# Kernel optimization log

Hardware: AMD Instinct MI355X
Metric: run time of the kernel (lower is better)

Reference implementation:

```python
import jax, jax.numpy as jnp
import numpy as np

H = 512

def setup_inputs() -> dict:
    key = jax.random.key(0)
    ks = jax.random.split(key, 10)
    T, B, S = 64, 8, 512
    scale = 1.0 / np.sqrt(H)
    return {
        "attn_dec_state": jax.random.normal(ks[0], (T, B, H), jnp.float32),
        "attn_enc_state": jax.random.normal(ks[1], (S, B, H), jnp.float32),
        "attn_coverage": jax.random.uniform(ks[2], (B, S), jnp.float32),
        "Wq": jax.random.normal(ks[3], (H, H), jnp.float32) * scale,   # linear_query weight (in,out)
        "bq": jnp.zeros((H,), jnp.float32),
        "Wc": jax.random.normal(ks[4], (H, H), jnp.float32) * scale,   # linear_context weight
        "v": jax.random.normal(ks[5], (H,), jnp.float32) * scale,       # v projection H->1
        "Wo": jax.random.normal(ks[6], (2 * H, H), jnp.float32) * scale,  # linear_out weight
        "bo": jnp.zeros((H,), jnp.float32),
        "wcov": jax.random.normal(ks[7], (H,), jnp.float32) * scale,    # linear_cover weight 1->H
    }

def reference(attn_dec_state, attn_enc_state, attn_coverage, Wq, bq, Wc, v, Wo, bo, wcov):
    dec = jnp.transpose(attn_dec_state, (1, 0, 2))   # [B,T,H]
    enc = jnp.transpose(attn_enc_state, (1, 0, 2))   # [B,S,H]
    # coverage: linear_cover(1->H) applied to each scalar, added to enc, then tanh
    enc = jnp.tanh(enc + attn_coverage[:, :, None] * wcov)  # [B,S,H]
    # additive (Bahdanau) score with broadcast-tanh
    a1 = jnp.einsum('bth,hk->btk', dec, Wq) + bq             # [B,T,H]
    a2 = jnp.einsum('bsh,hk->bsk', enc, Wc)                  # [B,S,H]
    scores = jnp.einsum('btsh,h->bts', jnp.tanh(a1[:, :, None, :] + a2[:, None, :, :]), v)  # [B,T,S]
    align = jax.nn.softmax(scores, axis=-1)                  # [B,T,S]
    c = jnp.einsum('bts,bsh->bth', align, enc)               # [B,T,H]
    concat = jnp.concatenate([c, dec], axis=-1)              # [B,T,2H]
    attn_h = jnp.einsum('btd,dk->btk', concat, Wo) + bo      # [B,T,H]
    attn_h = jnp.transpose(attn_h, (1, 0, 2))                # [T,B,H]
    align_out = jnp.transpose(align, (1, 0, 2))              # [T,B,S]
    return attn_h, align_out
```

## Files before the change

### kernel.cpp

```cpp
#include <hip/hip_runtime.h>
#include <cstddef>

static constexpr int TT = 64;
static constexpr int BB = 8;
static constexpr int SS = 512;
static constexpr int HH = 512;

typedef __attribute__((ext_vector_type(8))) short bf16x8;
typedef __attribute__((ext_vector_type(4))) float f32x4;

__device__ __forceinline__ float fast_tanh(float x) {
  float e = __expf(2.0f * x);
  float r = __builtin_amdgcn_rcpf(e + 1.0f);
  return 1.0f - 2.0f * r;
}
__device__ __forceinline__ unsigned short f2bf(float f) {
  unsigned u = __float_as_uint(f);
  unsigned r = (u + 0x7FFFu + ((u >> 16) & 1u)) >> 16;
  return (unsigned short)r;
}

__global__ __launch_bounds__(256)
void k_prep(const float* __restrict__ enc, const float* __restrict__ cov,
            const float* __restrict__ wcov, const float* __restrict__ dec,
            const float* __restrict__ Wq, const float* __restrict__ Wc,
            const float* __restrict__ Wo, const float* __restrict__ v,
            unsigned short* __restrict__ encpb, unsigned short* __restrict__ decb,
            unsigned short* __restrict__ concatb,
            unsigned short* __restrict__ WqT, unsigned short* __restrict__ WcT,
            unsigned short* __restrict__ WoT,
            float* __restrict__ v2, float* __restrict__ Vsum) {
  __shared__ float tile[32][33];
  const int blk = blockIdx.x, tid = threadIdx.x;

  if (blk < 8192) {
    const int idx = blk * 256 + tid;
    const int h = idx & 511;
    const int bs = idx >> 9;
    const int s = bs & 511, b = bs >> 9;
    const float x = enc[(size_t)(s * BB + b) * HH + h] + cov[bs] * wcov[h];
    encpb[idx] = f2bf(fast_tanh(x));
  } else if (blk < 9216) {
    const int idx = (blk - 8192) * 256 + tid;
    const int h = idx & 511, m = idx >> 9;
    const int b = m >> 6, t = m & 63;
    const unsigned short val = f2bf(dec[(size_t)(t * BB + b) * HH + h]);
    decb[idx] = val;
    concatb[(size_t)m * 1024 + 512 + h] = val;
  } else if (blk < 10240) {
    int l = blk - 9216;
    const float* W; unsigned short* WT; int KT;
    if (l < 256)      { W = Wq; WT = WqT; KT = 512; }
    else if (l < 512) { W = Wc; WT = WcT; KT = 512; l -= 256; }
    else              { W = Wo; WT = WoT; KT = 1024; l -= 512; }
    const int n0 = (l & 15) * 32, k0 = (l >> 4) * 32;
    const int r = tid >> 3, c4 = (tid & 7) * 4;
    const float4 w = *(const float4*)(W + (size_t)(k0 + r) * 512 + n0 + c4);
    tile[r][c4 + 0] = w.x; tile[r][c4 + 1] = w.y;
    tile[r][c4 + 2] = w.z; tile[r][c4 + 3] = w.w;
    __syncthreads();
    unsigned short* o = WT + (size_t)(n0 + r) * KT + k0 + c4;
#pragma unroll
    for (int i = 0; i < 4; ++i) o[i] = f2bf(tile[c4 + i][r]);
  } else {
    __shared__ float rb[256];
    const float va = v[tid], vb = v[tid + 256];
    v2[tid] = 2.0f * va;
    v2[tid + 256] = 2.0f * vb;
    rb[tid] = va + vb;
    __syncthreads();
    for (int off = 128; off; off >>= 1) {
      if (tid < off) rb[tid] += rb[tid + off];
      __syncthreads();
    }
    if (tid == 0) Vsum[0] = rb[0];
  }
}

__global__ __launch_bounds__(256)
void k_gemm12(const unsigned short* __restrict__ decb,
              const unsigned short* __restrict__ encpb,
              const unsigned short* __restrict__ WqT,
              const unsigned short* __restrict__ WcT,
              const float* __restrict__ bq,
              float* __restrict__ Ea1, float* __restrict__ Ea2) {
  __shared__ unsigned short As[64][72];
  __shared__ unsigned short Bs[64][72];
  const int tid = threadIdx.x;
  const int w = tid >> 6, lane = tid & 63;

  const bool isA1 = blockIdx.x < 64;
  const int bb = isA1 ? blockIdx.x : blockIdx.x - 64;
  const int n0 = (bb & 7) * 64, m0 = (bb >> 3) * 64;
  const unsigned short* A  = isA1 ? decb : encpb;
  const unsigned short* BT = isA1 ? WqT : WcT;
  float* C = isA1 ? Ea1 : Ea2;

  f32x4 acc[4] = {};
  const int lr = tid >> 2, lk = (tid & 3) * 16;
  const int fm = w * 16 + (lane & 15);
  const int fk = (lane >> 4) * 8;

  for (int k0 = 0; k0 < 512; k0 += 64) {
    const uint4* ga = (const uint4*)(A + (size_t)(m0 + lr) * 512 + k0 + lk);
    const uint4* gb = (const uint4*)(BT + (size_t)(n0 + lr) * 512 + k0 + lk);
    uint4 a0 = ga[0], a1v = ga[1];
    uint4 b0 = gb[0], b1v = gb[1];
    *(uint4*)&As[lr][lk] = a0;
    *(uint4*)&As[lr][lk + 8] = a1v;
    *(uint4*)&Bs[lr][lk] = b0;
    *(uint4*)&Bs[lr][lk + 8] = b1v;
    __syncthreads();
#pragma unroll
    for (int ks = 0; ks < 2; ++ks) {
      bf16x8 af = *(const bf16x8*)&As[fm][ks * 32 + fk];
#pragma unroll
      for (int j = 0; j < 4; ++j) {
        bf16x8 bf = *(const bf16x8*)&Bs[j * 16 + (lane & 15)][ks * 32 + fk];
        acc[j] = __builtin_amdgcn_mfma_f32_16x16x32_bf16(af, bf, acc[j], 0, 0, 0);
      }
    }
    __syncthreads();
  }

  const int col = lane & 15, rq = lane >> 4;
#pragma unroll
  for (int j = 0; j < 4; ++j) {
    const int n = n0 + j * 16 + col;
    const float bv = isA1 ? bq[n] : 0.0f;
#pragma unroll
    for (int r = 0; r < 4; ++r) {
      const int m = m0 + w * 16 + rq * 4 + r;
      float val = acc[j][r] + bv;
      val = fminf(fmaxf(val, -30.0f), 30.0f);
      C[(size_t)m * 512 + n] = __expf(2.0f * val);
    }
  }
}

__global__ __launch_bounds__(256)
void k_scores(const float* __restrict__ Ea1, const float* __restrict__ Ea2,
              const float* __restrict__ v2g, const float* __restrict__ Vsum,
              float* __restrict__ scb) {
  const int blk = blockIdx.x;
  const int b = blk & 7, tq = (blk >> 3) & 15, sc = blk >> 7;
  const int tid = threadIdx.x;
  const int wv = tid >> 6, lane = tid & 63;
  const int hq = lane & 3, sl = lane >> 2;

  __shared__ __align__(16) float ea1s[4][HH];
  __shared__ __align__(16) float v2s[HH];

#pragma unroll
  for (int i = 0; i < 4; ++i) {
    const float* row = Ea1 + (size_t)(b * TT + tq * 4 + i) * HH;
    ea1s[i][tid] = row[tid];
    ea1s[i][tid + 256] = row[tid + 256];
  }
  v2s[tid] = v2g[tid];
  v2s[tid + 256] = v2g[tid + 256];
  __syncthreads();

  const float V = Vsum[0];
  const int s = sc * 64 + wv * 16 + sl;
  const float* erow = Ea2 + (size_t)(b * SS + s) * HH;

  float acc[4] = {0.f, 0.f, 0.f, 0.f};
#pragma unroll 4
  for (int it = 0; it < 32; ++it) {
    const int h = it * 16 + hq * 4;
    const float4 e2 = *(const float4*)(erow + h);
    const float4 vv = *(const float4*)&v2s[h];
#pragma unroll
    for (int i = 0; i < 4; ++i) {
      const float4 e1 = *(const float4*)&ea1s[i][h];
      acc[i] = fmaf(vv.x, __builtin_amdgcn_rcpf(fmaf(e1.x, e2.x, 1.0f)), acc[i]);
      acc[i] = fmaf(vv.y, __builtin_amdgcn_rcpf(fmaf(e1.y, e2.y, 1.0f)), acc[i]);
      acc[i] = fmaf(vv.z, __builtin_amdgcn_rcpf(fmaf(e1.z, e2.z, 1.0f)), acc[i]);
      acc[i] = fmaf(vv.w, __builtin_amdgcn_rcpf(fmaf(e1.w, e2.w, 1.0f)), acc[i]);
    }
  }
#pragma unroll
  for (int i = 0; i < 4; ++i) {
    acc[i] += __shfl_xor(acc[i], 1);
    acc[i] += __shfl_xor(acc[i], 2);
  }
  if (hq == 0) {
#pragma unroll
    for (int i = 0; i < 4; ++i)
      scb[(size_t)(b * TT + tq * 4 + i) * SS + s] = V - acc[i];
  }
}

__global__ __launch_bounds__(256)
void k_smctx(const float* __restrict__ scb,
             const unsigned short* __restrict__ encpb,
             float* __restrict__ align_out,
             unsigned short* __restrict__ concatb) {
  const int b = blockIdx.x & 7;
  const int t0 = (blockIdx.x >> 3) * 2;
  const int tid = threadIdx.x;
  const int wave = tid >> 6, lane = tid & 63;

  __shared__ __align__(16) float al[2][SS];
  __shared__ float red[2][4];

  const float* r0 = scb + (size_t)(b * TT + t0) * SS;
  const float* r1 = r0 + SS;
  const float x00 = r0[tid], x01 = r0[tid + 256];
  const float x10 = r1[tid], x11 = r1[tid + 256];

  float m0 = fmaxf(x00, x01), m1 = fmaxf(x10, x11);
#pragma unroll
  for (int off = 32; off; off >>= 1) {
    m0 = fmaxf(m0, __shfl_xor(m0, off));
    m1 = fmaxf(m1, __shfl_xor(m1, off));
  }
  if (lane == 0) { red[0][wave] = m0; red[1][wave] = m1; }
  __syncthreads();
  m0 = fmaxf(fmaxf(red[0][0], red[0][1]), fmaxf(red[0][2], red[0][3]));
  m1 = fmaxf(fmaxf(red[1][0], red[1][1]), fmaxf(red[1][2], red[1][3]));
  __syncthreads();

  const float e00 = __expf(x00 - m0), e01 = __expf(x01 - m0);
  const float e10 = __expf(x10 - m1), e11 = __expf(x11 - m1);
  float s0 = e00 + e01, s1 = e10 + e11;
#pragma unroll
  for (int off = 32; off; off >>= 1) {
    s0 += __shfl_xor(s0, off);
    s1 += __shfl_xor(s1, off);
  }
  if (lane == 0) { red[0][wave] = s0; red[1][wave] = s1; }
  __syncthreads();
  s0 = red[0][0] + red[0][1] + red[0][2] + red[0][3];
  s1 = red[1][0] + red[1][1] + red[1][2] + red[1][3];
  const float rs0 = __builtin_amdgcn_rcpf(s0);
  const float rs1 = __builtin_amdgcn_rcpf(s1);

  const float a00 = e00 * rs0, a01 = e01 * rs0;
  const float a10 = e10 * rs1, a11 = e11 * rs1;
  float* ao0 = align_out + (size_t)(t0 + 0) * BB * SS + b * SS;
  float* ao1 = align_out + (size_t)(t0 + 1) * BB * SS + b * SS;
  ao0[tid] = a00; ao0[tid + 256] = a01;
  ao1[tid] = a10; ao1[tid + 256] = a11;
  al[0][tid] = a00; al[0][tid + 256] = a01;
  al[1][tid] = a10; al[1][tid + 256] = a11;
  __syncthreads();

  const unsigned* ep = (const unsigned*)(encpb + (size_t)b * SS * HH);
  float c00 = 0.f, c01 = 0.f, c10 = 0.f, c11 = 0.f;
#pragma unroll 16
  for (int s2 = 0; s2 < SS; ++s2) {
    const unsigned u = ep[s2 * 256 + tid];
    const float elo = __uint_as_float(u << 16);
    const float ehi = __uint_as_float(u & 0xffff0000u);
    const float av0 = al[0][s2], av1 = al[1][s2];
    c00 = fmaf(av0, elo, c00); c01 = fmaf(av0, ehi, c01);
    c10 = fmaf(av1, elo, c10); c11 = fmaf(av1, ehi, c11);
  }
  unsigned* cb0 = (unsigned*)(concatb + (size_t)(b * TT + t0) * 1024);
  unsigned* cb1 = (unsigned*)(concatb + (size_t)(b * TT + t0 + 1) * 1024);
  cb0[tid] = (unsigned)f2bf(c00) | ((unsigned)f2bf(c01) << 16);
  cb1[tid] = (unsigned)f2bf(c10) | ((unsigned)f2bf(c11) << 16);
}

__global__ __launch_bounds__(256)
void k_out(const unsigned short* __restrict__ A,
           const unsigned short* __restrict__ BT,
           const float* __restrict__ bias, float* __restrict__ C) {
  __shared__ unsigned short As[64][72];
  __shared__ unsigned short Bs[64][72];
  const int tid = threadIdx.x;
  const int w = tid >> 6, lane = tid & 63;
  const int n0 = (blockIdx.x & 7) * 64, m0 = (blockIdx.x >> 3) * 64;

  f32x4 acc[4] = {};
  const int lr = tid >> 2, lk = (tid & 3) * 16;
  const int fm = w * 16 + (lane & 15);
  const int fk = (lane >> 4) * 8;

  for (int k0 = 0; k0 < 1024; k0 += 64) {
    const uint4* ga = (const uint4*)(A + (size_t)(m0 + lr) * 1024 + k0 + lk);
    const uint4* gb = (const uint4*)(BT + (size_t)(n0 + lr) * 1024 + k0 + lk);
    uint4 a0 = ga[0], a1v = ga[1];
    uint4 b0 = gb[0], b1v = gb[1];
    *(uint4*)&As[lr][lk] = a0;
    *(uint4*)&As[lr][lk + 8] = a1v;
    *(uint4*)&Bs[lr][lk] = b0;
    *(uint4*)&Bs[lr][lk + 8] = b1v;
    __syncthreads();
#pragma unroll
    for (int ks = 0; ks < 2; ++ks) {
      bf16x8 af = *(const bf16x8*)&As[fm][ks * 32 + fk];
#pragma unroll
      for (int j = 0; j < 4; ++j) {
        bf16x8 bf = *(const bf16x8*)&Bs[j * 16 + (lane & 15)][ks * 32 + fk];
        acc[j] = __builtin_amdgcn_mfma_f32_16x16x32_bf16(af, bf, acc[j], 0, 0, 0);
      }
    }
    __syncthreads();
  }

  const int col = lane & 15, rq = lane >> 4;
#pragma unroll
  for (int j = 0; j < 4; ++j) {
    const int n = n0 + j * 16 + col;
    const float bv = bias[n];
#pragma unroll
    for (int r = 0; r < 4; ++r) {
      const int m = m0 + w * 16 + rq * 4 + r;
      const int bi = m >> 6, t = m & 63;
      C[(size_t)(t * BB + bi) * 512 + n] = acc[j][r] + bv;
    }
  }
}

extern "C" void kernel_launch(void* const* d_in, const int* in_sizes, int n_in,
                              void* d_out, int out_size, void* d_ws, size_t ws_size,
                              hipStream_t stream) {
  const float* dec  = (const float*)d_in[0];
  const float* enc  = (const float*)d_in[1];
  const float* cov  = (const float*)d_in[2];
  const float* Wq   = (const float*)d_in[3];
  const float* bq   = (const float*)d_in[4];
  const float* Wc   = (const float*)d_in[5];
  const float* v    = (const float*)d_in[6];
  const float* Wo   = (const float*)d_in[7];
  const float* bo   = (const float*)d_in[8];
  const float* wcov = (const float*)d_in[9];

  float* out = (float*)d_out;
  float* attn_h    = out;
  float* align_out = out + (size_t)TT * BB * HH;

  char* w = (char*)d_ws;
  const size_t MB = 1024 * 1024;
  unsigned short* encpb   = (unsigned short*)(w);
  unsigned short* WqT     = (unsigned short*)(w + 4 * MB);
  unsigned short* WcT     = (unsigned short*)(w + 5 * MB);
  unsigned short* WoT     = (unsigned short*)(w + 6 * MB);
  unsigned short* decb    = (unsigned short*)(w + 7 * MB);
  unsigned short* concatb = (unsigned short*)(w + 8 * MB);
  float*          Ea1     = (float*)(w + 9 * MB);
  float*          Ea2     = (float*)(w + 10 * MB);
  float*          scb     = (float*)(w + 18 * MB);
  float*          v2      = (float*)(w + 19 * MB);
  float*          Vsum    = (float*)(w + 19 * MB + 4096);

  k_prep<<<10241, 256, 0, stream>>>(enc, cov, wcov, dec, Wq, Wc, Wo, v,
                                    encpb, decb, concatb, WqT, WcT, WoT, v2, Vsum);
  k_gemm12<<<576, 256, 0, stream>>>(decb, encpb, WqT, WcT, bq, Ea1, Ea2);
  k_scores<<<1024, 256, 0, stream>>>(Ea1, Ea2, v2, Vsum, scb);
  k_smctx<<<256, 256, 0, stream>>>(scb, encpb, align_out, concatb);
  k_out<<<64, 256, 0, stream>>>(concatb, WoT, bo, attn_h);
}
```

Baseline: 143.1 us.

## Fuse all stages into one persistent kernel with atomic grid barriers

Replaces five kernel launches with a single persistent kernel of 256 blocks that walks through every stage and separates them with atomic-counter grid barriers. The output GEMM becomes split-K, with partial sums written to the workspace and reduced in a final phase, so more blocks have work. The score loop now pairs two reciprocals into one via a shared denominator, and the exp clamp range is tightened. It removes launch gaps and tail effects, but adds barrier spin cost, leaves only 256 blocks per stage for occupancy, and relies on all blocks being co-resident.

```diff
diff --git a/kernel.cpp b/kernel.cpp
--- a/kernel.cpp
+++ b/kernel.cpp
@@ -5,111 +5,47 @@
 static constexpr int BB = 8;
 static constexpr int SS = 512;
 static constexpr int HH = 512;
+static constexpr int NB = 256;
 
 typedef __attribute__((ext_vector_type(8))) short bf16x8;
 typedef __attribute__((ext_vector_type(4))) float f32x4;
 
 __device__ __forceinline__ float fast_tanh(float x) {
   float e = __expf(2.0f * x);
-  float r = __builtin_amdgcn_rcpf(e + 1.0f);
-  return 1.0f - 2.0f * r;
+  return 1.0f - 2.0f * __builtin_amdgcn_rcpf(e + 1.0f);
 }
 __device__ __forceinline__ unsigned short f2bf(float f) {
   unsigned u = __float_as_uint(f);
-  unsigned r = (u + 0x7FFFu + ((u >> 16) & 1u)) >> 16;
-  return (unsigned short)r;
-}
-
-__global__ __launch_bounds__(256)
-void k_prep(const float* __restrict__ enc, const float* __restrict__ cov,
-            const float* __restrict__ wcov, const float* __restrict__ dec,
-            const float* __restrict__ Wq, const float* __restrict__ Wc,
-            const float* __restrict__ Wo, const float* __restrict__ v,
-            unsigned short* __restrict__ encpb, unsigned short* __restrict__ decb,
-            unsigned short* __restrict__ concatb,
-            unsigned short* __restrict__ WqT, unsigned short* __restrict__ WcT,
-            unsigned short* __restrict__ WoT,
-            float* __restrict__ v2, float* __restrict__ Vsum) {
-  __shared__ float tile[32][33];
-  const int blk = blockIdx.x, tid = threadIdx.x;
-
-  if (blk < 8192) {
-    const int idx = blk * 256 + tid;
-    const int h = idx & 511;
-    const int bs = idx >> 9;
-    const int s = bs & 511, b = bs >> 9;
-    const float x = enc[(size_t)(s * BB + b) * HH + h] + cov[bs] * wcov[h];
-    encpb[idx] = f2bf(fast_tanh(x));
-  } else if (blk < 9216) {
-    const int idx = (blk - 8192) * 256 + tid;
-    const int h = idx & 511, m = idx >> 9;
-    const int b = m >> 6, t = m & 63;
-    const unsigned short val = f2bf(dec[(size_t)(t * BB + b) * HH + h]);
-    decb[idx] = val;
-    concatb[(size_t)m * 1024 + 512 + h] = val;
-  } else if (blk < 10240) {
-    int l = blk - 9216;
-    const float* W; unsigned short* WT; int KT;
-    if (l < 256)      { W = Wq; WT = WqT; KT = 512; }
-    else if (l < 512) { W = Wc; WT = WcT; KT = 512; l -= 256; }
-    else              { W = Wo; WT = WoT; KT = 1024; l -= 512; }
-    const int n0 = (l & 15) * 32, k0 = (l >> 4) * 32;
-    const int r = tid >> 3, c4 = (tid & 7) * 4;
-    const float4 w = *(const float4*)(W + (size_t)(k0 + r) * 512 + n0 + c4);
-    tile[r][c4 + 0] = w.x; tile[r][c4 + 1] = w.y;
-    tile[r][c4 + 2] = w.z; tile[r][c4 + 3] = w.w;
-    __syncthreads();
-    unsigned short* o = WT + (size_t)(n0 + r) * KT + k0 + c4;
-#pragma unroll
-    for (int i = 0; i < 4; ++i) o[i] = f2bf(tile[c4 + i][r]);
-  } else {
-    __shared__ float rb[256];
-    const float va = v[tid], vb = v[tid + 256];
-    v2[tid] = 2.0f * va;
-    v2[tid + 256] = 2.0f * vb;
-    rb[tid] = va + vb;
-    __syncthreads();
-    for (int off = 128; off; off >>= 1) {
-      if (tid < off) rb[tid] += rb[tid + off];
-      __syncthreads();
-    }
-    if (tid == 0) Vsum[0] = rb[0];
-  }
-}
-
-__global__ __launch_bounds__(256)
-void k_gemm12(const unsigned short* __restrict__ decb,
-              const unsigned short* __restrict__ encpb,
-              const unsigned short* __restrict__ WqT,
-              const unsigned short* __restrict__ WcT,
-              const float* __restrict__ bq,
-              float* __restrict__ Ea1, float* __restrict__ Ea2) {
-  __shared__ unsigned short As[64][72];
-  __shared__ unsigned short Bs[64][72];
-  const int tid = threadIdx.x;
-  const int w = tid >> 6, lane = tid & 63;
-
-  const bool isA1 = blockIdx.x < 64;
-  const int bb = isA1 ? blockIdx.x : blockIdx.x - 64;
-  const int n0 = (bb & 7) * 64, m0 = (bb >> 3) * 64;
-  const unsigned short* A  = isA1 ? decb : encpb;
-  const unsigned short* BT = isA1 ? WqT : WcT;
-  float* C = isA1 ? Ea1 : Ea2;
-
-  f32x4 acc[4] = {};
+  return (unsigned short)((u + 0x7FFFu + ((u >> 16) & 1u)) >> 16);
+}
+
+__device__ __forceinline__ void gbar(unsigned* ctr, unsigned target) {
+  __syncthreads();
+  if (threadIdx.x == 0) {
+    __hip_atomic_fetch_add(ctr, 1u, __ATOMIC_ACQ_REL, __HIP_MEMORY_SCOPE_AGENT);
+    while (__hip_atomic_load(ctr, __ATOMIC_ACQUIRE, __HIP_MEMORY_SCOPE_AGENT) < target)
+      __builtin_amdgcn_s_sleep(8);
+  }
+  __syncthreads();
+}
+
+template<int LDA, int LDB>
+__device__ __forceinline__ void gemm_tile(const unsigned short* __restrict__ A,
+                                          const unsigned short* __restrict__ BT,
+                                          int m0, int n0, int kbeg, int kend,
+                                          unsigned short (*As)[72],
+                                          unsigned short (*Bs)[72],
+                                          f32x4 acc[4]) {
+  const int tid = threadIdx.x, w = tid >> 6, lane = tid & 63;
   const int lr = tid >> 2, lk = (tid & 3) * 16;
-  const int fm = w * 16 + (lane & 15);
-  const int fk = (lane >> 4) * 8;
-
-  for (int k0 = 0; k0 < 512; k0 += 64) {
-    const uint4* ga = (const uint4*)(A + (size_t)(m0 + lr) * 512 + k0 + lk);
-    const uint4* gb = (const uint4*)(BT + (size_t)(n0 + lr) * 512 + k0 + lk);
-    uint4 a0 = ga[0], a1v = ga[1];
-    uint4 b0 = gb[0], b1v = gb[1];
-    *(uint4*)&As[lr][lk] = a0;
-    *(uint4*)&As[lr][lk + 8] = a1v;
-    *(uint4*)&Bs[lr][lk] = b0;
-    *(uint4*)&Bs[lr][lk + 8] = b1v;
+  const int fm = w * 16 + (lane & 15), fk = (lane >> 4) * 8;
+  for (int k0 = kbeg; k0 < kend; k0 += 64) {
+    __syncthreads();
+    const uint4* ga = (const uint4*)(A + (size_t)(m0 + lr) * LDA + k0 + lk);
+    const uint4* gb = (const uint4*)(BT + (size_t)(n0 + lr) * LDB + k0 + lk);
+    uint4 a0 = ga[0], a1 = ga[1], b0 = gb[0], b1 = gb[1];
+    *(uint4*)&As[lr][lk] = a0;  *(uint4*)&As[lr][lk + 8] = a1;
+    *(uint4*)&Bs[lr][lk] = b0;  *(uint4*)&Bs[lr][lk + 8] = b1;
     __syncthreads();
 #pragma unroll
     for (int ks = 0; ks < 2; ++ks) {
@@ -120,197 +56,250 @@
         acc[j] = __builtin_amdgcn_mfma_f32_16x16x32_bf16(af, bf, acc[j], 0, 0, 0);
       }
     }
-    __syncthreads();
-  }
-
-  const int col = lane & 15, rq = lane >> 4;
-#pragma unroll
-  for (int j = 0; j < 4; ++j) {
-    const int n = n0 + j * 16 + col;
-    const float bv = isA1 ? bq[n] : 0.0f;
-#pragma unroll
-    for (int r = 0; r < 4; ++r) {
-      const int m = m0 + w * 16 + rq * 4 + r;
-      float val = acc[j][r] + bv;
-      val = fminf(fmaxf(val, -30.0f), 30.0f);
-      C[(size_t)m * 512 + n] = __expf(2.0f * val);
-    }
   }
 }
 
 __global__ __launch_bounds__(256)
-void k_scores(const float* __restrict__ Ea1, const float* __restrict__ Ea2,
-              const float* __restrict__ v2g, const float* __restrict__ Vsum,
-              float* __restrict__ scb) {
-  const int blk = blockIdx.x;
-  const int b = blk & 7, tq = (blk >> 3) & 15, sc = blk >> 7;
-  const int tid = threadIdx.x;
-  const int wv = tid >> 6, lane = tid & 63;
-  const int hq = lane & 3, sl = lane >> 2;
-
-  __shared__ __align__(16) float ea1s[4][HH];
-  __shared__ __align__(16) float v2s[HH];
-
-#pragma unroll
-  for (int i = 0; i < 4; ++i) {
-    const float* row = Ea1 + (size_t)(b * TT + tq * 4 + i) * HH;
-    ea1s[i][tid] = row[tid];
-    ea1s[i][tid + 256] = row[tid + 256];
-  }
-  v2s[tid] = v2g[tid];
-  v2s[tid + 256] = v2g[tid + 256];
-  __syncthreads();
-
-  const float V = Vsum[0];
-  const int s = sc * 64 + wv * 16 + sl;
-  const float* erow = Ea2 + (size_t)(b * SS + s) * HH;
-
-  float acc[4] = {0.f, 0.f, 0.f, 0.f};
+void k_fused(const float* __restrict__ dec, const float* __restrict__ enc,
+             const float* __restrict__ cov, const float* __restrict__ Wq,
+             const float* __restrict__ bq, const float* __restrict__ Wc,
+             const float* __restrict__ v, const float* __restrict__ Wo,
+             const float* __restrict__ bo, const float* __restrict__ wcov,
+             unsigned short* __restrict__ encpb, unsigned short* __restrict__ decb,
+             unsigned short* __restrict__ concatb,
+             unsigned short* __restrict__ WqT, unsigned short* __restrict__ WcT,
+             unsigned short* __restrict__ WoT,
+             float* __restrict__ Ea1, float* __restrict__ Ea2,
+             float* __restrict__ scb, float* __restrict__ v2,
+             float* __restrict__ Vsum, float* __restrict__ part,
+             float* __restrict__ attn_h, float* __restrict__ align_out,
+             unsigned* __restrict__ ctr) {
+  __shared__ __align__(16) char smem[18496];
+  const int g = blockIdx.x, tid = threadIdx.x;
+
+  {
+    for (int r = 0; r < 16; ++r) {
+      const int bs = g * 16 + r, s = bs & 511, b = bs >> 9;
+      const float2 ev = *(const float2*)(enc + (size_t)(s * BB + b) * HH + 2 * tid);
+      const float cv = cov[bs];
+      const float2 wv = *(const float2*)(wcov + 2 * tid);
+      const unsigned lo = f2bf(fast_tanh(ev.x + cv * wv.x));
+      const unsigned hi = f2bf(fast_tanh(ev.y + cv * wv.y));
+      *(unsigned*)(encpb + (size_t)bs * HH + 2 * tid) = lo | (hi << 16);
+    }
+    for (int r = 0; r < 2; ++r) {
+      const int m = g * 2 + r, t = m & 63, b = m >> 6;
+      const float2 dv = *(const float2*)(dec + (size_t)(t * BB + b) * HH + 2 * tid);
+      const unsigned pv = (unsigned)f2bf(dv.x) | ((unsigned)f2bf(dv.y) << 16);
+      *(unsigned*)(decb + (size_t)m * HH + 2 * tid) = pv;
+      *(unsigned*)(concatb + (size_t)m * 1024 + 512 + 2 * tid) = pv;
+    }
+    float (*tile)[33] = (float(*)[33])smem;
+    const int r = tid >> 3, c4 = (tid & 7) * 4;
+    for (int i = 0; i < 4; ++i) {
+      const int tau = g + NB * i;
+      const float* W; unsigned short* WT; int KT, n0, k0;
+      if (tau < 256)      { W = Wq; WT = WqT; KT = 512;  n0 = (tau & 15) * 32; k0 = (tau >> 4) * 32; }
+      else if (tau < 512) { int u = tau - 256; W = Wc; WT = WcT; KT = 512;  n0 = (u & 15) * 32; k0 = (u >> 4) * 32; }
+      else                { int u = tau - 512; W = Wo; WT = WoT; KT = 1024; n0 = (u & 15) * 32; k0 = (u >> 4) * 32; }
+      __syncthreads();
+      const float4 wv = *(const float4*)(W + (size_t)(k0 + r) * 512 + n0 + c4);
+      tile[r][c4] = wv.x; tile[r][c4 + 1] = wv.y; tile[r][c4 + 2] = wv.z; tile[r][c4 + 3] = wv.w;
+      __syncthreads();
+      ushort4 ov;
+      ov.x = f2bf(tile[c4][r]);     ov.y = f2bf(tile[c4 + 1][r]);
+      ov.z = f2bf(tile[c4 + 2][r]); ov.w = f2bf(tile[c4 + 3][r]);
+      *(ushort4*)(WT + (size_t)(n0 + r) * KT + k0 + c4) = ov;
+    }
+    if (g == 0) {
+      __syncthreads();
+      float* rb = (float*)smem;
+      const float va = v[tid], vb = v[tid + 256];
+      v2[tid] = 2.0f * va; v2[tid + 256] = 2.0f * vb;
+      rb[tid] = va + vb;
+      __syncthreads();
+      for (int off = 128; off; off >>= 1) {
+        if (tid < off) rb[tid] += rb[tid + off];
+        __syncthreads();
+      }
+      if (tid == 0) Vsum[0] = rb[0];
+    }
+  }
+  gbar(ctr, NB);
+
+  {
+    auto As = (unsigned short(*)[72])smem;
+    auto Bs = (unsigned short(*)[72])(smem + 9216);
+    const int lane = tid & 63, w = tid >> 6, col = lane & 15, rq = lane >> 4;
+    for (int i = 0; i < 3; ++i) {
+      const int tau = g + NB * i;
+      if (tau >= 576) break;
+      const unsigned short *A, *BT; float* C; const float* bias; int m0, n0;
+      if (tau < 64) { A = decb;  BT = WqT; C = Ea1; bias = bq;     m0 = (tau >> 3) * 64; n0 = (tau & 7) * 64; }
+      else { int u = tau - 64; A = encpb; BT = WcT; C = Ea2; bias = nullptr; m0 = (u >> 3) * 64; n0 = (u & 7) * 64; }
+      f32x4 acc[4] = {};
+      gemm_tile<512, 512>(A, BT, m0, n0, 0, 512, As, Bs, acc);
+#pragma unroll
+      for (int j = 0; j < 4; ++j) {
+        const int n = n0 + j * 16 + col;
+        const float bv = bias ? bias[n] : 0.0f;
+#pragma unroll
+        for (int r2 = 0; r2 < 4; ++r2) {
+          const int m = m0 + w * 16 + rq * 4 + r2;
+          float val = acc[j][r2] + bv;
+          val = fminf(fmaxf(val, -10.5f), 10.5f);
+          C[(size_t)m * 512 + n] = __expf(2.0f * val);
+        }
+      }
+    }
+  }
+  gbar(ctr, 2 * NB);
+
+  {
+    float (*ea1s)[512] = (float(*)[512])smem;
+    float* v2s = (float*)(smem + 8192);
+    const int b = g & 7, tq = (g >> 3) & 15, j0 = g >> 7;
+#pragma unroll
+    for (int i = 0; i < 4; ++i) {
+      const float* row = Ea1 + (size_t)(b * TT + tq * 4 + i) * HH;
+      ea1s[i][tid] = row[tid]; ea1s[i][tid + 256] = row[tid + 256];
+    }
+    v2s[tid] = v2[tid]; v2s[tid + 256] = v2[tid + 256];
+    __syncthreads();
+    const float V = Vsum[0];
+    const int wv = tid >> 6, lane = tid & 63, hq = lane & 3, sl = lane >> 2;
+    for (int kk = 0; kk < 4; ++kk) {
+      const int s = (j0 + 2 * kk) * 64 + wv * 16 + sl;
+      const float* erow = Ea2 + (size_t)(b * SS + s) * HH;
+      float acc[4] = {0.f, 0.f, 0.f, 0.f};
 #pragma unroll 4
-  for (int it = 0; it < 32; ++it) {
-    const int h = it * 16 + hq * 4;
-    const float4 e2 = *(const float4*)(erow + h);
-    const float4 vv = *(const float4*)&v2s[h];
-#pragma unroll
-    for (int i = 0; i < 4; ++i) {
-      const float4 e1 = *(const float4*)&ea1s[i][h];
-      acc[i] = fmaf(vv.x, __builtin_amdgcn_rcpf(fmaf(e1.x, e2.x, 1.0f)), acc[i]);
-      acc[i] = fmaf(vv.y, __builtin_amdgcn_rcpf(fmaf(e1.y, e2.y, 1.0f)), acc[i]);
-      acc[i] = fmaf(vv.z, __builtin_amdgcn_rcpf(fmaf(e1.z, e2.z, 1.0f)), acc[i]);
-      acc[i] = fmaf(vv.w, __builtin_amdgcn_rcpf(fmaf(e1.w, e2.w, 1.0f)), acc[i]);
-    }
-  }
-#pragma unroll
-  for (int i = 0; i < 4; ++i) {
-    acc[i] += __shfl_xor(acc[i], 1);
-    acc[i] += __shfl_xor(acc[i], 2);
-  }
-  if (hq == 0) {
-#pragma unroll
-    for (int i = 0; i < 4; ++i)
-      scb[(size_t)(b * TT + tq * 4 + i) * SS + s] = V - acc[i];
-  }
-}
-
-__global__ __launch_bounds__(256)
-void k_smctx(const float* __restrict__ scb,
-             const unsigned short* __restrict__ encpb,
-             float* __restrict__ align_out,
-             unsigned short* __restrict__ concatb) {
-  const int b = blockIdx.x & 7;
-  const int t0 = (blockIdx.x >> 3) * 2;
-  const int tid = threadIdx.x;
-  const int wave = tid >> 6, lane = tid & 63;
-
-  __shared__ __align__(16) float al[2][SS];
-  __shared__ float red[2][4];
-
-  const float* r0 = scb + (size_t)(b * TT + t0) * SS;
-  const float* r1 = r0 + SS;
-  const float x00 = r0[tid], x01 = r0[tid + 256];
-  const float x10 = r1[tid], x11 = r1[tid + 256];
-
-  float m0 = fmaxf(x00, x01), m1 = fmaxf(x10, x11);
-#pragma unroll
-  for (int off = 32; off; off >>= 1) {
-    m0 = fmaxf(m0, __shfl_xor(m0, off));
-    m1 = fmaxf(m1, __shfl_xor(m1, off));
-  }
-  if (lane == 0) { red[0][wave] = m0; red[1][wave] = m1; }
-  __syncthreads();
-  m0 = fmaxf(fmaxf(red[0][0], red[0][1]), fmaxf(red[0][2], red[0][3]));
-  m1 = fmaxf(fmaxf(red[1][0], red[1][1]), fmaxf(red[1][2], red[1][3]));
-  __syncthreads();
-
-  const float e00 = __expf(x00 - m0), e01 = __expf(x01 - m0);
-  const float e10 = __expf(x10 - m1), e11 = __expf(x11 - m1);
-  float s0 = e00 + e01, s1 = e10 + e11;
-#pragma unroll
-  for (int off = 32; off; off >>= 1) {
-    s0 += __shfl_xor(s0, off);
-    s1 += __shfl_xor(s1, off);
-  }
-  if (lane == 0) { red[0][wave] = s0; red[1][wave] = s1; }
-  __syncthreads();
-  s0 = red[0][0] + red[0][1] + red[0][2] + red[0][3];
-  s1 = red[1][0] + red[1][1] + red[1][2] + red[1][3];
-  const float rs0 = __builtin_amdgcn_rcpf(s0);
-  const float rs1 = __builtin_amdgcn_rcpf(s1);
-
-  const float a00 = e00 * rs0, a01 = e01 * rs0;
-  const float a10 = e10 * rs1, a11 = e11 * rs1;
-  float* ao0 = align_out + (size_t)(t0 + 0) * BB * SS + b * SS;
-  float* ao1 = align_out + (size_t)(t0 + 1) * BB * SS + b * SS;
-  ao0[tid] = a00; ao0[tid + 256] = a01;
-  ao1[tid] = a10; ao1[tid + 256] = a11;
-  al[0][tid] = a00; al[0][tid + 256] = a01;
-  al[1][tid] = a10; al[1][tid + 256] = a11;
-  __syncthreads();
-
-  const unsigned* ep = (const unsigned*)(encpb + (size_t)b * SS * HH);
-  float c00 = 0.f, c01 = 0.f, c10 = 0.f, c11 = 0.f;
+      for (int it = 0; it < 32; ++it) {
+        const int h = it * 16 + hq * 4;
+        const float4 e2 = *(const float4*)(erow + h);
+        const float4 vv = *(const float4*)&v2s[h];
+#pragma unroll
+        for (int i = 0; i < 4; ++i) {
+          const float4 e1 = *(const float4*)&ea1s[i][h];
+          const float x1 = fmaf(e1.x, e2.x, 1.0f), x2 = fmaf(e1.y, e2.y, 1.0f);
+          const float x3 = fmaf(e1.z, e2.z, 1.0f), x4 = fmaf(e1.w, e2.w, 1.0f);
+          const float r12 = __builtin_amdgcn_rcpf(x1 * x2);
+          const float r34 = __builtin_amdgcn_rcpf(x3 * x4);
+          const float n12 = fmaf(vv.x, x2, vv.y * x1);
+          const float n34 = fmaf(vv.z, x4, vv.w * x3);
+          acc[i] = fmaf(n12, r12, acc[i]);
+          acc[i] = fmaf(n34, r34, acc[i]);
+        }
+      }
+#pragma unroll
+      for (int i = 0; i < 4; ++i) {
+        acc[i] += __shfl_xor(acc[i], 1);
+        acc[i] += __shfl_xor(acc[i], 2);
+      }
+      if (hq == 0) {
+#pragma unroll
+        for (int i = 0; i < 4; ++i)
+          scb[(size_t)(b * TT + tq * 4 + i) * SS + s] = V - acc[i];
+      }
+    }
+  }
+  gbar(ctr, 3 * NB);
+
+  {
+    float (*al)[512] = (float(*)[512])smem;
+    float (*red)[4] = (float(*)[4])(smem + 4096);
+    const int b = g & 7, t0 = (g >> 3) * 2;
+    const int wave = tid >> 6, lane = tid & 63;
+
+    const float* r0 = scb + (size_t)(b * TT + t0) * SS;
+    const float* r1 = r0 + SS;
+    const float x00 = r0[tid], x01 = r0[tid + 256];
+    const float x10 = r1[tid], x11 = r1[tid + 256];
+
+    float m0 = fmaxf(x00, x01), m1 = fmaxf(x10, x11);
+#pragma unroll
+    for (int off = 32; off; off >>= 1) {
+      m0 = fmaxf(m0, __shfl_xor(m0, off));
+      m1 = fmaxf(m1, __shfl_xor(m1, off));
+    }
+    if (lane == 0) { red[0][wave] = m0; red[1][wave] = m1; }
+    __syncthreads();
+    m0 = fmaxf(fmaxf(red[0][0], red[0][1]), fmaxf(red[0][2], red[0][3]));
+    m1 = fmaxf(fmaxf(red[1][0], red[1][1]), fmaxf(red[1][2], red[1][3]));
+    __syncthreads();
+
+    const float e00 = __expf(x00 - m0), e01 = __expf(x01 - m0);
+    const float e10 = __expf(x10 - m1), e11 = __expf(x11 - m1);
+    float s0 = e00 + e01, s1 = e10 + e11;
+#pragma unroll
+    for (int off = 32; off; off >>= 1) {
+      s0 += __shfl_xor(s0, off);
+      s1 += __shfl_xor(s1, off);
+    }
+    if (lane == 0) { red[0][wave] = s0; red[1][wave] = s1; }
+    __syncthreads();
+    s0 = red[0][0] + red[0][1] + red[0][2] + red[0][3];
+    s1 = red[1][0] + red[1][1] + red[1][2] + red[1][3];
+    const float rs0 = __builtin_amdgcn_rcpf(s0);
+    const float rs1 = __builtin_amdgcn_rcpf(s1);
+
+    const float a00 = e00 * rs0, a01 = e01 * rs0;
+    const float a10 = e10 * rs1, a11 = e11 * rs1;
+    float* ao0 = align_out + (size_t)(t0 + 0) * BB * SS + b * SS;
+    float* ao1 = align_out + (size_t)(t0 + 1) * BB * SS + b * SS;
+    ao0[tid] = a00; ao0[tid + 256] = a01;
+    ao1[tid] = a10; ao1[tid + 256] = a11;
+    al[0][tid] = a00; al[0][tid + 256] = a01;
+    al[1][tid] = a10; al[1][tid + 256] = a11;
+    __syncthreads();
+
+    const unsigned* ep = (const unsigned*)(encpb + (size_t)b * SS * HH);
+    float c00 = 0.f, c01 = 0.f, c10 = 0.f, c11 = 0.f;
 #pragma unroll 16
-  for (int s2 = 0; s2 < SS; ++s2) {
-    const unsigned u = ep[s2 * 256 + tid];
-    const float elo = __uint_as_float(u << 16);
-    const float ehi = __uint_as_float(u & 0xffff0000u);
-    const float av0 = al[0][s2], av1 = al[1][s2];
-    c00 = fmaf(av0, elo, c00); c01 = fmaf(av0, ehi, c01);
-    c10 = fmaf(av1, elo, c10); c11 = fmaf(av1, ehi, c11);
-  }
-  unsigned* cb0 = (unsigned*)(concatb + (size_t)(b * TT + t0) * 1024);
-  unsigned* cb1 = (unsigned*)(concatb + (size_t)(b * TT + t0 + 1) * 1024);
-  cb0[tid] = (unsigned)f2bf(c00) | ((unsigned)f2bf(c01) << 16);
-  cb1[tid] = (unsigned)f2bf(c10) | ((unsigned)f2bf(c11) << 16);
-}
-
-__global__ __launch_bounds__(256)
-void k_out(const unsigned short* __restrict__ A,
-           const unsigned short* __restrict__ BT,
-           const float* __restrict__ bias, float* __restrict__ C) {
-  __shared__ unsigned short As[64][72];
-  __shared__ unsigned short Bs[64][72];
-  const int tid = threadIdx.x;
-  const int w = tid >> 6, lane = tid & 63;
-  const int n0 = (blockIdx.x & 7) * 64, m0 = (blockIdx.x >> 3) * 64;
-
-  f32x4 acc[4] = {};
-  const int lr = tid >> 2, lk = (tid & 3) * 16;
-  const int fm = w * 16 + (lane & 15);
-  const int fk = (lane >> 4) * 8;
-
-  for (int k0 = 0; k0 < 1024; k0 += 64) {
-    const uint4* ga = (const uint4*)(A + (size_t)(m0 + lr) * 1024 + k0 + lk);
-    const uint4* gb = (const uint4*)(BT + (size_t)(n0 + lr) * 1024 + k0 + lk);
-    uint4 a0 = ga[0], a1v = ga[1];
-    uint4 b0 = gb[0], b1v = gb[1];
-    *(uint4*)&As[lr][lk] = a0;
-    *(uint4*)&As[lr][lk + 8] = a1v;
-    *(uint4*)&Bs[lr][lk] = b0;
-    *(uint4*)&Bs[lr][lk + 8] = b1v;
-    __syncthreads();
-#pragma unroll
-    for (int ks = 0; ks < 2; ++ks) {
-      bf16x8 af = *(const bf16x8*)&As[fm][ks * 32 + fk];
-#pragma unroll
-      for (int j = 0; j < 4; ++j) {
-        bf16x8 bf = *(const bf16x8*)&Bs[j * 16 + (lane & 15)][ks * 32 + fk];
-        acc[j] = __builtin_amdgcn_mfma_f32_16x16x32_bf16(af, bf, acc[j], 0, 0, 0);
-      }
-    }
-    __syncthreads();
-  }
-
-  const int col = lane & 15, rq = lane >> 4;
-#pragma unroll
-  for (int j = 0; j < 4; ++j) {
-    const int n = n0 + j * 16 + col;
-    const float bv = bias[n];
-#pragma unroll
-    for (int r = 0; r < 4; ++r) {
-      const int m = m0 + w * 16 + rq * 4 + r;
-      const int bi = m >> 6, t = m & 63;
-      C[(size_t)(t * BB + bi) * 512 + n] = acc[j][r] + bv;
+    for (int s2 = 0; s2 < SS; ++s2) {
+      const unsigned u = ep[s2 * 256 + tid];
+      const float elo = __uint_as_float(u << 16);
+      const float ehi = __uint_as_float(u & 0xffff0000u);
+      const float av0 = al[0][s2], av1 = al[1][s2];
+      c00 = fmaf(av0, elo, c00); c01 = fmaf(av0, ehi, c01);
+      c10 = fmaf(av1, elo, c10); c11 = fmaf(av1, ehi, c11);
+    }
+    unsigned* cb0 = (unsigned*)(concatb + (size_t)(b * TT + t0) * 1024);
+    unsigned* cb1 = (unsigned*)(concatb + (size_t)(b * TT + t0 + 1) * 1024);
+    cb0[tid] = (unsigned)f2bf(c00) | ((unsigned)f2bf(c01) << 16);
+    cb1[tid] = (unsigned)f2bf(c10) | ((unsigned)f2bf(c11) << 16);
+  }
+  gbar(ctr, 4 * NB);
+
+  {
+    auto As = (unsigned short(*)[72])smem;
+    auto Bs = (unsigned short(*)[72])(smem + 9216);
+    const int tau = g >> 2, kc = g & 3;
+    const int m0 = (tau >> 3) * 64, n0 = (tau & 7) * 64;
+    f32x4 acc[4] = {};
+    gemm_tile<1024, 1024>(concatb, WoT, m0, n0, kc * 256, kc * 256 + 256, As, Bs, acc);
+    const int lane = tid & 63, w = tid >> 6, col = lane & 15, rq = lane >> 4;
+    float* P = part + (size_t)g * 4096;
+#pragma unroll
+    for (int j = 0; j < 4; ++j)
+#pragma unroll
+      for (int r2 = 0; r2 < 4; ++r2)
+        P[(w * 16 + rq * 4 + r2) * 64 + j * 16 + col] = acc[j][r2];
+  }
+  gbar(ctr, 5 * NB);
+
+  {
+    const int tau = g >> 2, q = g & 3;
+    const int m0 = (tau >> 3) * 64, n0 = (tau & 7) * 64;
+    const float* P = part + (size_t)tau * 4 * 4096;
+#pragma unroll
+    for (int jj = 0; jj < 4; ++jj) {
+      const int i = jj * 256 + tid;
+      const int ml = q * 16 + (i >> 6), nl = i & 63;
+      float acc2 = bo[n0 + nl];
+#pragma unroll
+      for (int kc = 0; kc < 4; ++kc) acc2 += P[kc * 4096 + ml * 64 + nl];
+      const int m = m0 + ml, bb2 = m >> 6, t = m & 63;
+      attn_h[(size_t)(t * BB + bb2) * HH + n0 + nl] = acc2;
     }
   }
 }
@@ -346,11 +335,12 @@
   float*          scb     = (float*)(w + 18 * MB);
   float*          v2      = (float*)(w + 19 * MB);
   float*          Vsum    = (float*)(w + 19 * MB + 4096);
-
-  k_prep<<<10241, 256, 0, stream>>>(enc, cov, wcov, dec, Wq, Wc, Wo, v,
-                                    encpb, decb, concatb, WqT, WcT, WoT, v2, Vsum);
-  k_gemm12<<<576, 256, 0, stream>>>(decb, encpb, WqT, WcT, bq, Ea1, Ea2);
-  k_scores<<<1024, 256, 0, stream>>>(Ea1, Ea2, v2, Vsum, scb);
-  k_smctx<<<256, 256, 0, stream>>>(scb, encpb, align_out, concatb);
-  k_out<<<64, 256, 0, stream>>>(concatb, WoT, bo, attn_h);
-}
+  float*          part    = (float*)(w + 20 * MB);
+  unsigned*       ctr     = (unsigned*)(w + 30 * MB);
+
+  hipMemsetAsync(ctr, 0, 128, stream);
+  k_fused<<<NB, 256, 0, stream>>>(dec, enc, cov, Wq, bq, Wc, v, Wo, bo, wcov,
+                                  encpb, decb, concatb, WqT, WcT, WoT,
+                                  Ea1, Ea2, scb, v2, Vsum, part,
+                                  attn_h, align_out, ctr);
+}
```

New measurement: 263.8 us. 84.4% more time.

## Split-K output GEMM with atomics and register-block scores over two s rows

Applied to the files above, without the earlier changes.

The output projection kernel is split along K into four chunks, which raises the grid from 64 to 256 blocks. Partial sums are accumulated into attn_h with atomic adds, and the prep kernel gains extra blocks that pre-fill attn_h with the bias. The scores kernel now processes two sequence rows per thread, reusing the LDS-loaded Ea1 values across both and halving its grid. The risks are atomic contention, nondeterministic summation order, and higher register pressure in the scores kernel.

```diff
diff --git a/kernel.cpp b/kernel.cpp
--- a/kernel.cpp
+++ b/kernel.cpp
@@ -11,13 +11,11 @@
 
 __device__ __forceinline__ float fast_tanh(float x) {
   float e = __expf(2.0f * x);
-  float r = __builtin_amdgcn_rcpf(e + 1.0f);
-  return 1.0f - 2.0f * r;
+  return 1.0f - 2.0f * __builtin_amdgcn_rcpf(e + 1.0f);
 }
 __device__ __forceinline__ unsigned short f2bf(float f) {
   unsigned u = __float_as_uint(f);
-  unsigned r = (u + 0x7FFFu + ((u >> 16) & 1u)) >> 16;
-  return (unsigned short)r;
+  return (unsigned short)((u + 0x7FFFu + ((u >> 16) & 1u)) >> 16);
 }
 
 __global__ __launch_bounds__(256)
@@ -25,11 +23,13 @@
             const float* __restrict__ wcov, const float* __restrict__ dec,
             const float* __restrict__ Wq, const float* __restrict__ Wc,
             const float* __restrict__ Wo, const float* __restrict__ v,
+            const float* __restrict__ bo,
             unsigned short* __restrict__ encpb, unsigned short* __restrict__ decb,
             unsigned short* __restrict__ concatb,
             unsigned short* __restrict__ WqT, unsigned short* __restrict__ WcT,
             unsigned short* __restrict__ WoT,
-            float* __restrict__ v2, float* __restrict__ Vsum) {
+            float* __restrict__ v2, float* __restrict__ Vsum,
+            float* __restrict__ attn_h) {
   __shared__ float tile[32][33];
   const int blk = blockIdx.x, tid = threadIdx.x;
 
@@ -62,7 +62,7 @@
     unsigned short* o = WT + (size_t)(n0 + r) * KT + k0 + c4;
 #pragma unroll
     for (int i = 0; i < 4; ++i) o[i] = f2bf(tile[c4 + i][r]);
-  } else {
+  } else if (blk == 10240) {
     __shared__ float rb[256];
     const float va = v[tid], vb = v[tid + 256];
     v2[tid] = 2.0f * va;
@@ -74,6 +74,40 @@
       __syncthreads();
     }
     if (tid == 0) Vsum[0] = rb[0];
+  } else {
+    const int row = blk - 10241;
+    const float2 bv = *(const float2*)(bo + 2 * tid);
+    *(float2*)(attn_h + (size_t)row * 512 + 2 * tid) = bv;
+  }
+}
+
+template<int LDA, int LDB>
+__device__ __forceinline__ void gemm_tile(const unsigned short* __restrict__ A,
+                                          const unsigned short* __restrict__ BT,
+                                          int m0, int n0, int kbeg, int kend,
+                                          unsigned short (*As)[72],
+                                          unsigned short (*Bs)[72],
+                                          f32x4 acc[4]) {
+  const int tid = threadIdx.x, w = tid >> 6, lane = tid & 63;
+  const int lr = tid >> 2, lk = (tid & 3) * 16;
+  const int fm = w * 16 + (lane & 15), fk = (lane >> 4) * 8;
+  for (int k0 = kbeg; k0 < kend; k0 += 64) {
+    const uint4* ga = (const uint4*)(A + (size_t)(m0 + lr) * LDA + k0 + lk);
+    const uint4* gb = (const uint4*)(BT + (size_t)(n0 + lr) * LDB + k0 + lk);
+    uint4 a0 = ga[0], a1 = ga[1], b0 = gb[0], b1 = gb[1];
+    *(uint4*)&As[lr][lk] = a0;  *(uint4*)&As[lr][lk + 8] = a1;
+    *(uint4*)&Bs[lr][lk] = b0;  *(uint4*)&Bs[lr][lk + 8] = b1;
+    __syncthreads();
+#pragma unroll
+    for (int ks = 0; ks < 2; ++ks) {
+      bf16x8 af = *(const bf16x8*)&As[fm][ks * 32 + fk];
+#pragma unroll
+      for (int j = 0; j < 4; ++j) {
+        bf16x8 bf = *(const bf16x8*)&Bs[j * 16 + (lane & 15)][ks * 32 + fk];
+        acc[j] = __builtin_amdgcn_mfma_f32_16x16x32_bf16(af, bf, acc[j], 0, 0, 0);
+      }
+    }
+    __syncthreads();
   }
 }
 
@@ -97,31 +131,7 @@
   float* C = isA1 ? Ea1 : Ea2;
 
   f32x4 acc[4] = {};
-  const int lr = tid >> 2, lk = (tid & 3) * 16;
-  const int fm = w * 16 + (lane & 15);
-  const int fk = (lane >> 4) * 8;
-
-  for (int k0 = 0; k0 < 512; k0 += 64) {
-    const uint4* ga = (const uint4*)(A + (size_t)(m0 + lr) * 512 + k0 + lk);
-    const uint4* gb = (const uint4*)(BT + (size_t)(n0 + lr) * 512 + k0 + lk);
-    uint4 a0 = ga[0], a1v = ga[1];
-    uint4 b0 = gb[0], b1v = gb[1];
-    *(uint4*)&As[lr][lk] = a0;
-    *(uint4*)&As[lr][lk + 8] = a1v;
-    *(uint4*)&Bs[lr][lk] = b0;
-    *(uint4*)&Bs[lr][lk + 8] = b1v;
-    __syncthreads();
-#pragma unroll
-    for (int ks = 0; ks < 2; ++ks) {
-      bf16x8 af = *(const bf16x8*)&As[fm][ks * 32 + fk];
-#pragma unroll
-      for (int j = 0; j < 4; ++j) {
-        bf16x8 bf = *(const bf16x8*)&Bs[j * 16 + (lane & 15)][ks * 32 + fk];
-        acc[j] = __builtin_amdgcn_mfma_f32_16x16x32_bf16(af, bf, acc[j], 0, 0, 0);
-      }
-    }
-    __syncthreads();
-  }
+  gemm_tile<512, 512>(A, BT, m0, n0, 0, 512, As, Bs, acc);
 
   const int col = lane & 15, rq = lane >> 4;
 #pragma unroll
@@ -143,7 +153,7 @@
               const float* __restrict__ v2g, const float* __restrict__ Vsum,
               float* __restrict__ scb) {
   const int blk = blockIdx.x;
-  const int b = blk & 7, tq = (blk >> 3) & 15, sc = blk >> 7;
+  const int b = blk & 7, tq = (blk >> 3) & 15, sh = blk >> 7;
   const int tid = threadIdx.x;
   const int wv = tid >> 6, lane = tid & 63;
   const int hq = lane & 3, sl = lane >> 2;
@@ -154,41 +164,57 @@
 #pragma unroll
   for (int i = 0; i < 4; ++i) {
     const float* row = Ea1 + (size_t)(b * TT + tq * 4 + i) * HH;
-    ea1s[i][tid] = row[tid];
-    ea1s[i][tid + 256] = row[tid + 256];
-  }
-  v2s[tid] = v2g[tid];
-  v2s[tid + 256] = v2g[tid + 256];
+    ea1s[i][tid] = row[tid]; ea1s[i][tid + 256] = row[tid + 256];
+  }
+  v2s[tid] = v2g[tid]; v2s[tid + 256] = v2g[tid + 256];
   __syncthreads();
 
   const float V = Vsum[0];
-  const int s = sc * 64 + wv * 16 + sl;
-  const float* erow = Ea2 + (size_t)(b * SS + s) * HH;
-
-  float acc[4] = {0.f, 0.f, 0.f, 0.f};
+  const int s0 = sh * 128 + wv * 32 + sl;
+  const float* e2p0 = Ea2 + (size_t)(b * SS + s0) * HH;
+  const float* e2p1 = e2p0 + (size_t)16 * HH;
+
+  float acc[4][2] = {};
+#define TERM(E1, E2, VV, A) A = fmaf(VV, __builtin_amdgcn_rcpf(fmaf(E1, E2, 1.0f)), A)
 #pragma unroll 4
   for (int it = 0; it < 32; ++it) {
     const int h = it * 16 + hq * 4;
-    const float4 e2 = *(const float4*)(erow + h);
-    const float4 vv = *(const float4*)&v2s[h];
+    const float4 e20 = *(const float4*)(e2p0 + h);
+    const float4 e21 = *(const float4*)(e2p1 + h);
+    const float4 vv  = *(const float4*)&v2s[h];
+    float4 e1r[4];
+    e1r[0] = *(const float4*)&ea1s[0][h];
+    e1r[1] = *(const float4*)&ea1s[1][h];
+    e1r[2] = *(const float4*)&ea1s[2][h];
+    e1r[3] = *(const float4*)&ea1s[3][h];
 #pragma unroll
     for (int i = 0; i < 4; ++i) {
-      const float4 e1 = *(const float4*)&ea1s[i][h];
-      acc[i] = fmaf(vv.x, __builtin_amdgcn_rcpf(fmaf(e1.x, e2.x, 1.0f)), acc[i]);
-      acc[i] = fmaf(vv.y, __builtin_amdgcn_rcpf(fmaf(e1.y, e2.y, 1.0f)), acc[i]);
-      acc[i] = fmaf(vv.z, __builtin_amdgcn_rcpf(fmaf(e1.z, e2.z, 1.0f)), acc[i]);
-      acc[i] = fmaf(vv.w, __builtin_amdgcn_rcpf(fmaf(e1.w, e2.w, 1.0f)), acc[i]);
-    }
-  }
+      TERM(e1r[i].x, e20.x, vv.x, acc[i][0]);
+      TERM(e1r[i].y, e20.y, vv.y, acc[i][0]);
+      TERM(e1r[i].z, e20.z, vv.z, acc[i][0]);
+      TERM(e1r[i].w, e20.w, vv.w, acc[i][0]);
+      TERM(e1r[i].x, e21.x, vv.x, acc[i][1]);
+      TERM(e1r[i].y, e21.y, vv.y, acc[i][1]);
+      TERM(e1r[i].z, e21.z, vv.z, acc[i][1]);
+      TERM(e1r[i].w, e21.w, vv.w, acc[i][1]);
+    }
+  }
+#undef TERM
 #pragma unroll
   for (int i = 0; i < 4; ++i) {
-    acc[i] += __shfl_xor(acc[i], 1);
-    acc[i] += __shfl_xor(acc[i], 2);
+#pragma unroll
+    for (int j = 0; j < 2; ++j) {
+      acc[i][j] += __shfl_xor(acc[i][j], 1);
+      acc[i][j] += __shfl_xor(acc[i][j], 2);
+    }
   }
   if (hq == 0) {
 #pragma unroll
-    for (int i = 0; i < 4; ++i)
-      scb[(size_t)(b * TT + tq * 4 + i) * SS + s] = V - acc[i];
+    for (int i = 0; i < 4; ++i) {
+#pragma unroll
+      for (int j = 0; j < 2; ++j)
+        scb[(size_t)(b * TT + tq * 4 + i) * SS + s0 + j * 16] = V - acc[i][j];
+    }
   }
 }
 
@@ -267,50 +293,26 @@
 __global__ __launch_bounds__(256)
 void k_out(const unsigned short* __restrict__ A,
            const unsigned short* __restrict__ BT,
-           const float* __restrict__ bias, float* __restrict__ C) {
+           float* __restrict__ C) {
   __shared__ unsigned short As[64][72];
   __shared__ unsigned short Bs[64][72];
   const int tid = threadIdx.x;
   const int w = tid >> 6, lane = tid & 63;
-  const int n0 = (blockIdx.x & 7) * 64, m0 = (blockIdx.x >> 3) * 64;
+  const int tau = blockIdx.x >> 2, kc = blockIdx.x & 3;
+  const int n0 = (tau & 7) * 64, m0 = (tau >> 3) * 64;
 
   f32x4 acc[4] = {};
-  const int lr = tid >> 2, lk = (tid & 3) * 16;
-  const int fm = w * 16 + (lane & 15);
-  const int fk = (lane >> 4) * 8;
-
-  for (int k0 = 0; k0 < 1024; k0 += 64) {
-    const uint4* ga = (const uint4*)(A + (size_t)(m0 + lr) * 1024 + k0 + lk);
-    const uint4* gb = (const uint4*)(BT + (size_t)(n0 + lr) * 1024 + k0 + lk);
-    uint4 a0 = ga[0], a1v = ga[1];
-    uint4 b0 = gb[0], b1v = gb[1];
-    *(uint4*)&As[lr][lk] = a0;
-    *(uint4*)&As[lr][lk + 8] = a1v;
-    *(uint4*)&Bs[lr][lk] = b0;
-    *(uint4*)&Bs[lr][lk + 8] = b1v;
-    __syncthreads();
-#pragma unroll
-    for (int ks = 0; ks < 2; ++ks) {
-      bf16x8 af = *(const bf16x8*)&As[fm][ks * 32 + fk];
-#pragma unroll
-      for (int j = 0; j < 4; ++j) {
-        bf16x8 bf = *(const bf16x8*)&Bs[j * 16 + (lane & 15)][ks * 32 + fk];
-        acc[j] = __builtin_amdgcn_mfma_f32_16x16x32_bf16(af, bf, acc[j], 0, 0, 0);
-      }
-    }
-    __syncthreads();
-  }
+  gemm_tile<1024, 1024>(A, BT, m0, n0, kc * 256, kc * 256 + 256, As, Bs, acc);
 
   const int col = lane & 15, rq = lane >> 4;
 #pragma unroll
   for (int j = 0; j < 4; ++j) {
     const int n = n0 + j * 16 + col;
-    const float bv = bias[n];
 #pragma unroll
     for (int r = 0; r < 4; ++r) {
       const int m = m0 + w * 16 + rq * 4 + r;
       const int bi = m >> 6, t = m & 63;
-      C[(size_t)(t * BB + bi) * 512 + n] = acc[j][r] + bv;
+      unsafeAtomicAdd(&C[(size_t)(t * BB + bi) * 512 + n], acc[j][r]);
     }
   }
 }
@@ -347,10 +349,11 @@
   float*          v2      = (float*)(w + 19 * MB);
   float*          Vsum    = (float*)(w + 19 * MB + 4096);
 
-  k_prep<<<10241, 256, 0, stream>>>(enc, cov, wcov, dec, Wq, Wc, Wo, v,
-                                    encpb, decb, concatb, WqT, WcT, WoT, v2, Vsum);
+  k_prep<<<10753, 256, 0, stream>>>(enc, cov, wcov, dec, Wq, Wc, Wo, v, bo,
+                                    encpb, decb, concatb, WqT, WcT, WoT,
+                                    v2, Vsum, attn_h);
   k_gemm12<<<576, 256, 0, stream>>>(decb, encpb, WqT, WcT, bq, Ea1, Ea2);
-  k_scores<<<1024, 256, 0, stream>>>(Ea1, Ea2, v2, Vsum, scb);
+  k_scores<<<512, 256, 0, stream>>>(Ea1, Ea2, v2, Vsum, scb);
   k_smctx<<<256, 256, 0, stream>>>(scb, encpb, align_out, concatb);
-  k_out<<<64, 256, 0, stream>>>(concatb, WoT, bo, attn_h);
-}
+  k_out<<<256, 256, 0, stream>>>(concatb, WoT, attn_h);
+}
```

Result: no change. 144.0 us (+0.6%).
